# Kernel tuning notes

Measured on AMD Instinct MI355X. Metric: run time of the kernel, lower is better.

The kernel has to match this reference:

```python
import jax, jax.numpy as jnp
import numpy as np

N_EMBD = 1024
N_HEAD = 16
HEAD_SIZE = N_EMBD // N_HEAD


def setup_inputs() -> dict:
    key = jax.random.key(0)
    k_x, k_w, k_b = jax.random.split(key, 3)
    B, T, C = 2, 2048, N_EMBD
    x = jax.random.normal(k_x, (B, T, C), dtype=jnp.float32)
    # Linear(n_embd, 3*n_embd): weight [C, 3C] (applied as x @ W), bias [3C]
    w_qkv = jax.random.normal(k_w, (C, 3 * C), dtype=jnp.float32) * (1.0 / np.sqrt(C))
    b_qkv = jax.random.normal(k_b, (3 * C,), dtype=jnp.float32) * 0.02
    return {"x": x, "w_qkv": w_qkv, "b_qkv": b_qkv}


def reference(x, w_qkv, b_qkv):
    B, T, C = x.shape
    H, D = N_HEAD, HEAD_SIZE
    qkv = x @ w_qkv + b_qkv                      # [B, T, 3C]
    q, k, v = jnp.split(qkv, 3, axis=-1)         # each [B, T, C]
    # [B, T, C] -> [B, H, T, D]
    q = q.reshape(B, T, H, D).transpose(0, 2, 1, 3)
    k = k.reshape(B, T, H, D).transpose(0, 2, 1, 3)
    v = v.reshape(B, T, H, D).transpose(0, 2, 1, 3)
    scores = jnp.einsum('bhqd,bhkd->bhqk', q, k) / jnp.sqrt(jnp.float32(D))
    causal = jnp.tril(jnp.ones((T, T), dtype=bool))  # allow j <= i
    scores = jnp.where(causal[None, None, :, :], scores, -jnp.inf)
    weights = jax.nn.softmax(scores, axis=-1)    # [B, H, T, T]
    out = jnp.einsum('bhqk,bhkd->bhqd', weights, v)
    out = out.transpose(0, 2, 1, 3).reshape(B, T, C)
    return out
```

## Files before the change

### kernel.cpp

```cpp
#include <hip/hip_runtime.h>
#include <hip/hip_bf16.h>


#define CDIM  1024
#define C3    3072
#define HS    64
#define TLEN  2048
#define KVT   64
#define SCL   0.1803368801111204f

typedef __attribute__((ext_vector_type(8))) short bf16x8;
typedef __attribute__((ext_vector_type(4))) float f32x4;
typedef __attribute__((ext_vector_type(4))) unsigned short u16x4;

__device__ __forceinline__ unsigned short f2b(float f) {
    unsigned u = __float_as_uint(f);
    unsigned r = (u + 0x7FFFu + ((u >> 16) & 1u)) >> 16;
    return (unsigned short)r;
}
__device__ __forceinline__ float b2f(unsigned short u) {
    return __uint_as_float(((unsigned)u) << 16);
}
__device__ __forceinline__ float fexp2(float x) {
    return __builtin_amdgcn_exp2f(x);
}
__device__ __forceinline__ unsigned pkbf(float a, float b) {
    float2 f; f.x = a; f.y = b;
    __hip_bfloat162 h = __float22bfloat162_rn(f);
    union { __hip_bfloat162 h2; unsigned u; } c;
    c.h2 = h;
    return c.u;
}
__device__ __forceinline__ void gl_lds16(const unsigned short* g, unsigned short* l) {
    __builtin_amdgcn_global_load_lds((const __attribute__((address_space(1))) void*)g,
                                     (__attribute__((address_space(3))) void*)l, 16, 0, 0);
}
__device__ __forceinline__ int detect_bf(const void* bias, int lane) {
    unsigned w = ((const unsigned*)bias)[lane];
    unsigned e = (w >> 7) & 0xFF;
    unsigned long long m = __ballot(e >= 100 && e <= 135);
    return __popcll(m) >= 48;
}

__device__ __forceinline__ void plswap(unsigned x, unsigned& y0, unsigned& y1) {
    unsigned aa = x, bb = x;
    asm("v_permlane32_swap_b32 %0, %1" : "+v"(aa), "+v"(bb));
    asm("v_permlane16_swap_b32 %0, %1" : "+v"(aa), "+v"(bb));
    y0 = aa; y1 = bb;
}
__device__ __forceinline__ bf16x8 xfrag(unsigned x00, unsigned x01,
                                        unsigned x10, unsigned x11, int qsel) {
    unsigned y000, y100, y001, y101, y010, y110, y011, y111;
    plswap(x00, y000, y100);
    plswap(x01, y001, y101);
    plswap(x10, y010, y110);
    plswap(x11, y011, y111);
    union { unsigned u[4]; bf16x8 v; } r;
    r.u[0] = qsel ? y010 : y000;
    r.u[1] = qsel ? y011 : y001;
    r.u[2] = qsel ? y110 : y100;
    r.u[3] = qsel ? y111 : y101;
    return r.v;
}

__global__ __launch_bounds__(256) void k_prep(const void* __restrict__ w,
                                              const void* __restrict__ x,
                                              const void* __restrict__ bias,
                                              unsigned short* __restrict__ wt,
                                              unsigned short* __restrict__ xb) {
    __shared__ unsigned short tile[64 * 66];
    int t = threadIdx.x;
    int isbf = detect_bf(bias, t & 63);
    int bid = blockIdx.x;

    {
        int n0 = (bid % 48) * 64;
        int k0 = (bid / 48) * 64;
        for (int i = 0; i < 16; ++i) {
            int idx = t + i * 256;
            int r = idx >> 6, c = idx & 63;
            unsigned short v;
            if (isbf) v = ((const unsigned short*)w)[(k0 + r) * C3 + n0 + c];
            else      v = f2b(((const float*)w)[(k0 + r) * C3 + n0 + c]);
            tile[r * 66 + c] = v;
        }
        __syncthreads();
        for (int i = 0; i < 16; ++i) {
            int idx = t + i * 256;
            int r = idx >> 6, c = idx & 63;
            wt[(n0 + r) * CDIM + k0 + c] = tile[c * 66 + r];
        }
    }
    if (!isbf) {
        const float4* s = (const float4*)x;
        uint2* d = (uint2*)xb;
        for (int sb = bid; sb < 2048; sb += 768) {
            int base = sb * 512;
            for (int j = t; j < 512; j += 256) {
                float4 v = s[base + j];
                uint2 o_;
                o_.x = (unsigned)f2b(v.x) | ((unsigned)f2b(v.y) << 16);
                o_.y = (unsigned)f2b(v.z) | ((unsigned)f2b(v.w) << 16);
                d[base + j] = o_;
            }
        }
    }
}

__global__ __launch_bounds__(256, 3) void k_gemm_qkv(const void* __restrict__ xraw,
                                                     const unsigned short* __restrict__ xb,
                                                     const void* __restrict__ biasraw,
                                                     const unsigned short* __restrict__ Bt,
                                                     unsigned short* __restrict__ qk,
                                                     unsigned short* __restrict__ k2,
                                                     unsigned short* __restrict__ v2) {
    __shared__ __align__(16) unsigned short As[2 * 128 * 32];
    __shared__ __align__(16) unsigned short Bs[2 * 128 * 32];
    int tid  = threadIdx.x;
    int lane = tid & 63, wv = tid >> 6;
    int quad = lane >> 4, l16 = lane & 15;
    int isbf = detect_bf(biasraw, lane);
    const unsigned short* A = isbf ? (const unsigned short*)xraw : xb;

    int lin = blockIdx.x + 24 * blockIdx.y;
    int swz = (lin & 7) * 96 + (lin >> 3);
    int m0 = (swz / 24) * 128, n0 = (swz % 24) * 128;
    int wm = (wv >> 1) * 64, wn = (wv & 1) * 64;

    f32x4 acc[4][4] = {};

    int r0 = tid >> 2;
    int g0 = (((tid & 3) ^ (r0 & 3)) * 8);
    const unsigned short* a0 = A  + (m0 + r0) * CDIM + g0;
    const unsigned short* b0 = Bt + (n0 + r0) * CDIM + g0;
    unsigned short* dA = As + tid * 8;
    unsigned short* dB = Bs + tid * 8;

    int sw4 = l16 & 3;
    int aro = (wm + l16) * 32 + ((quad ^ sw4) * 8);
    int bro = (wn + l16) * 32 + ((quad ^ sw4) * 8);

    gl_lds16(a0,                 dA);
    gl_lds16(a0 + 64 * CDIM,     dA + 2048);
    gl_lds16(b0,                 dB);
    gl_lds16(b0 + 64 * CDIM,     dB + 2048);
    gl_lds16(a0 + 32,            dA + 4096);
    gl_lds16(a0 + 64 * CDIM + 32, dA + 4096 + 2048);
    gl_lds16(b0 + 32,            dB + 4096);
    gl_lds16(b0 + 64 * CDIM + 32, dB + 4096 + 2048);
    asm volatile("s_waitcnt vmcnt(4)" ::: "memory");
    __builtin_amdgcn_s_barrier();

    #pragma unroll 2
    for (int kt = 0; kt < 32; ++kt) {
        int cur = kt & 1;
        const unsigned short* Ac = As + cur * 4096;
        const unsigned short* Bc = Bs + cur * 4096;

        bf16x8 af[4], bfv[4];
        #pragma unroll
        for (int mt = 0; mt < 4; ++mt)
            af[mt] = *(const bf16x8*)&Ac[aro + mt * 512];
        #pragma unroll
        for (int nt = 0; nt < 4; ++nt)
            bfv[nt] = *(const bf16x8*)&Bc[bro + nt * 512];

        __builtin_amdgcn_s_setprio(1);
        #pragma unroll
        for (int mt = 0; mt < 4; ++mt)
            #pragma unroll
            for (int nt = 0; nt < 4; ++nt)
                acc[mt][nt] = __builtin_amdgcn_mfma_f32_16x16x32_bf16(af[mt], bfv[nt], acc[mt][nt], 0, 0, 0);
        __builtin_amdgcn_s_setprio(0);

        __builtin_amdgcn_s_barrier();
        if (kt < 30) {
            int koff = (kt + 2) * 32;
            unsigned short* tA = As + cur * 4096;
            unsigned short* tB = Bs + cur * 4096;
            gl_lds16(a0 + koff,            tA + tid * 8);
            gl_lds16(a0 + 64 * CDIM + koff, tA + tid * 8 + 2048);
            gl_lds16(b0 + koff,            tB + tid * 8);
            gl_lds16(b0 + 64 * CDIM + koff, tB + tid * 8 + 2048);
            asm volatile("s_waitcnt vmcnt(4)" ::: "memory");
        } else {
            asm volatile("s_waitcnt vmcnt(0)" ::: "memory");
        }
        __builtin_amdgcn_s_barrier();
    }

    if (n0 < 1024) {
        for (int mt = 0; mt < 4; ++mt) {
            int row = m0 + wm + mt * 16 + quad * 4;
            for (int nt = 0; nt < 4; ++nt) {
                int col = n0 + wn + nt * 16 + l16;
                float bv = isbf ? b2f(((const unsigned short*)biasraw)[col])
                                : ((const float*)biasraw)[col];
                for (int i = 0; i < 4; ++i)
                    qk[(row + i) * 2048 + col] = f2b(acc[mt][nt][i] + bv);
            }
        }
    } else if (n0 < 2048) {
        for (int mt = 0; mt < 4; ++mt) {
            int row = m0 + wm + mt * 16 + quad * 4;
            int tq = row & 2047, b = row >> 11;
            for (int nt = 0; nt < 4; ++nt) {
                int col = n0 + wn + nt * 16 + l16;
                float bv = isbf ? b2f(((const unsigned short*)biasraw)[col])
                                : ((const float*)biasraw)[col];
                int c = col - 1024;
                int hh = c >> 6, d = c & 63;
                int base = ((b * 16 + hh) * 32 + (tq >> 6)) * 4096
                         + ((tq >> 5) & 1) * 2048 + ((tq >> 4) & 1) * 1024
                         + (d >> 5) * 512 + ((d >> 3) & 3) * 128
                         + (tq & 15) * 8 + (d & 7);
                for (int i = 0; i < 4; ++i)
                    k2[base + i * 8] = f2b(acc[mt][nt][i] + bv);
            }
        }
    } else {
        for (int mt = 0; mt < 4; ++mt) {
            int row = m0 + wm + mt * 16 + quad * 4;
            int tq = row & 2047, b = row >> 11;
            for (int nt = 0; nt < 4; ++nt) {
                int col = n0 + wn + nt * 16 + l16;
                float bv = isbf ? b2f(((const unsigned short*)biasraw)[col])
                                : ((const float*)biasraw)[col];
                int c = col - 2048;
                int hh = c >> 6, d = c & 63;
                int base = ((b * 16 + hh) * 32 + (tq >> 6)) * 4096
                         + ((tq >> 5) & 1) * 2048 + (d >> 4) * 512
                         + ((tq >> 3) & 3) * 128 + (d & 15) * 8 + (tq & 7);
                u16x4 pk;
                for (int i = 0; i < 4; ++i) pk[i] = f2b(acc[mt][nt][i] + bv);
                *(u16x4*)&v2[base] = pk;
            }
        }
    }
}

__global__ __launch_bounds__(256, 3) void k_attn(const unsigned short* __restrict__ qk,
                                                 const unsigned short* __restrict__ k2,
                                                 const unsigned short* __restrict__ v2,
                                                 const void* __restrict__ biasraw,
                                                 void* __restrict__ outv) {
    __shared__ __align__(16) float SMf[4416];

    int tid  = threadIdx.x;
    int lane = tid & 63, wv = tid >> 6;
    int quad = lane >> 4, l16 = lane & 15;
    int isbf = detect_bf(biasraw, lane);
    int bh = blockIdx.x;
    int g  = 31 - blockIdx.y;
    int b = bh >> 4, h = bh & 15;
    int rowbase = b * TLEN;

    int s_ = wv >> 1;
    int p  = wv & 1;
    int qbase = 64 * g + 32 * s_;
    int T  = g + 1;
    int Tw = T - ((s_ == 0 && p == 1) ? 1 : 0);
    bool dmw = (p == s_);

    bf16x8 qf[2][2];
    for (int qt = 0; qt < 2; ++qt)
        for (int kh = 0; kh < 2; ++kh)
            qf[qt][kh] = *(const bf16x8*)&qk[(rowbase + qbase + qt * 16 + l16) * 2048
                                            + h * HS + kh * 32 + quad * 8];

    f32x4 o[2][4] = {};
    float ls[2] = {0.f, 0.f};

    const unsigned short* kp = k2 + bh * 131072 + p * 2048 + lane * 8;
    const unsigned short* vp = v2 + bh * 131072 + p * 2048 + lane * 8;

    bf16x8 kf00, kf01, kf10, kf11;
    f32x4 svA[2][2], svB[2][2];
    {
        bf16x8 k0a = *(const bf16x8*)kp;
        bf16x8 k0b = *(const bf16x8*)(kp + 512);
        bf16x8 k0c = *(const bf16x8*)(kp + 1024);
        bf16x8 k0d = *(const bf16x8*)(kp + 1536);
        kp += 4096;
        kf00 = *(const bf16x8*)kp;
        kf01 = *(const bf16x8*)(kp + 512);
        kf10 = *(const bf16x8*)(kp + 1024);
        kf11 = *(const bf16x8*)(kp + 1536);
        kp += 4096;
        #pragma unroll
        for (int qt = 0; qt < 2; ++qt) {
            f32x4 z0 = {};
            z0 = __builtin_amdgcn_mfma_f32_16x16x32_bf16(k0a, qf[qt][0], z0, 0, 0, 0);
            z0 = __builtin_amdgcn_mfma_f32_16x16x32_bf16(k0b, qf[qt][1], z0, 0, 0, 0);
            svA[qt][0] = z0;
            f32x4 z1 = {};
            z1 = __builtin_amdgcn_mfma_f32_16x16x32_bf16(k0c, qf[qt][0], z1, 0, 0, 0);
            z1 = __builtin_amdgcn_mfma_f32_16x16x32_bf16(k0d, qf[qt][1], z1, 0, 0, 0);
            svA[qt][1] = z1;
        }
    }

    auto trip = [&](f32x4 (&svin)[2][2], f32x4 (&svout)[2][2], int tt) {
        bf16x8 av0 = *(const bf16x8*)vp;
        bf16x8 av1 = *(const bf16x8*)(vp + 512);
        bf16x8 av2 = *(const bf16x8*)(vp + 1024);
        bf16x8 av3 = *(const bf16x8*)(vp + 1536);
        vp += 4096;

        __builtin_amdgcn_s_setprio(1);
        #pragma unroll
        for (int qt = 0; qt < 2; ++qt) {
            f32x4 z0 = {};
            z0 = __builtin_amdgcn_mfma_f32_16x16x32_bf16(kf00, qf[qt][0], z0, 0, 0, 0);
            z0 = __builtin_amdgcn_mfma_f32_16x16x32_bf16(kf01, qf[qt][1], z0, 0, 0, 0);
            svout[qt][0] = z0;
            f32x4 z1 = {};
            z1 = __builtin_amdgcn_mfma_f32_16x16x32_bf16(kf10, qf[qt][0], z1, 0, 0, 0);
            z1 = __builtin_amdgcn_mfma_f32_16x16x32_bf16(kf11, qf[qt][1], z1, 0, 0, 0);
            svout[qt][1] = z1;
        }
        __builtin_amdgcn_s_setprio(0);

        kf00 = *(const bf16x8*)kp;
        kf01 = *(const bf16x8*)(kp + 512);
        kf10 = *(const bf16x8*)(kp + 1024);
        kf11 = *(const bf16x8*)(kp + 1536);
        kp += 4096;

        unsigned sp[2][2][2];
        int kvb = tt * KVT + 32 * p;
        if (dmw && tt == T - 1) {
            #pragma unroll
            for (int qt = 0; qt < 2; ++qt) {
                float psum = 0.f;
                int q = qbase + qt * 16 + l16;
                #pragma unroll
                for (int nt = 0; nt < 2; ++nt) {
                    float pv[4];
                    #pragma unroll
                    for (int i = 0; i < 4; ++i) {
                        float arg = fmaf(svin[qt][nt][i], SCL, -12.0f);
                        int kv = kvb + nt * 16 + quad * 4 + i;
                        if (kv > q) arg = -1e30f;
                        pv[i] = fexp2(arg);
                        psum += pv[i];
                    }
                    sp[qt][nt][0] = pkbf(pv[0], pv[1]);
                    sp[qt][nt][1] = pkbf(pv[2], pv[3]);
                }
                ls[qt] += psum;
            }
        } else {
            #pragma unroll
            for (int qt = 0; qt < 2; ++qt) {
                float psum = 0.f;
                #pragma unroll
                for (int nt = 0; nt < 2; ++nt) {
                    float pv[4];
                    #pragma unroll
                    for (int i = 0; i < 4; ++i) {
                        float arg = fmaf(svin[qt][nt][i], SCL, -12.0f);
                        pv[i] = fexp2(arg);
                        psum += pv[i];
                    }
                    sp[qt][nt][0] = pkbf(pv[0], pv[1]);
                    sp[qt][nt][1] = pkbf(pv[2], pv[3]);
                }
                ls[qt] += psum;
            }
        }

        int qsel = quad & 2;
        bf16x8 f0 = xfrag(sp[0][0][0], sp[0][0][1], sp[0][1][0], sp[0][1][1], qsel);
        bf16x8 f1 = xfrag(sp[1][0][0], sp[1][0][1], sp[1][1][0], sp[1][1][1], qsel);
        __builtin_amdgcn_s_setprio(1);
        o[0][0] = __builtin_amdgcn_mfma_f32_16x16x32_bf16(av0, f0, o[0][0], 0, 0, 0);
        o[1][0] = __builtin_amdgcn_mfma_f32_16x16x32_bf16(av0, f1, o[1][0], 0, 0, 0);
        o[0][1] = __builtin_amdgcn_mfma_f32_16x16x32_bf16(av1, f0, o[0][1], 0, 0, 0);
        o[1][1] = __builtin_amdgcn_mfma_f32_16x16x32_bf16(av1, f1, o[1][1], 0, 0, 0);
        o[0][2] = __builtin_amdgcn_mfma_f32_16x16x32_bf16(av2, f0, o[0][2], 0, 0, 0);
        o[1][2] = __builtin_amdgcn_mfma_f32_16x16x32_bf16(av2, f1, o[1][2], 0, 0, 0);
        o[0][3] = __builtin_amdgcn_mfma_f32_16x16x32_bf16(av3, f0, o[0][3], 0, 0, 0);
        o[1][3] = __builtin_amdgcn_mfma_f32_16x16x32_bf16(av3, f1, o[1][3], 0, 0, 0);
        __builtin_amdgcn_s_setprio(0);
    };

    int t = 0;
    for (; t + 2 <= Tw; t += 2) {
        trip(svA, svB, t);
        trip(svB, svA, t + 1);
    }
    if (t < Tw) trip(svA, svB, t);

    #pragma unroll
    for (int qt = 0; qt < 2; ++qt) {
        ls[qt] += __shfl_xor(ls[qt], 16);
        ls[qt] += __shfl_xor(ls[qt], 32);
    }
    float* mrg  = SMf;
    float* lbuf = SMf + 4352;

    if (p == 1) {
        #pragma unroll
        for (int qt = 0; qt < 2; ++qt)
            #pragma unroll
            for (int dt = 0; dt < 4; ++dt)
                *(f32x4*)&mrg[s_ * (32 * 68) + (qt * 16 + l16) * 68 + dt * 16 + quad * 4] = o[qt][dt];
        if (quad == 0) {
            lbuf[s_ * 32 + l16]      = ls[0];
            lbuf[s_ * 32 + 16 + l16] = ls[1];
        }
    }
    __syncthreads();
    if (p == 0) {
        #pragma unroll
        for (int qt = 0; qt < 2; ++qt) {
            float lt = ls[qt] + lbuf[s_ * 32 + qt * 16 + l16];
            float inv = 1.0f / lt;
            int q = qbase + qt * 16 + l16;
            if (isbf) {
                unsigned short* out = (unsigned short*)outv;
                #pragma unroll
                for (int dt = 0; dt < 4; ++dt) {
                    f32x4 m = *(const f32x4*)&mrg[s_ * (32 * 68) + (qt * 16 + l16) * 68 + dt * 16 + quad * 4];
                    u16x4 ov;
                    #pragma unroll
                    for (int i = 0; i < 4; ++i) ov[i] = f2b((o[qt][dt][i] + m[i]) * inv);
                    *(u16x4*)&out[(rowbase + q) * CDIM + h * HS + dt * 16 + quad * 4] = ov;
                }
            } else {
                float* out = (float*)outv;
                #pragma unroll
                for (int dt = 0; dt < 4; ++dt) {
                    f32x4 m = *(const f32x4*)&mrg[s_ * (32 * 68) + (qt * 16 + l16) * 68 + dt * 16 + quad * 4];
                    float4 ov;
                    ov.x = (o[qt][dt][0] + m[0]) * inv;
                    ov.y = (o[qt][dt][1] + m[1]) * inv;
                    ov.z = (o[qt][dt][2] + m[2]) * inv;
                    ov.w = (o[qt][dt][3] + m[3]) * inv;
                    *(float4*)&out[(rowbase + q) * CDIM + h * HS + dt * 16 + quad * 4] = ov;
                }
            }
        }
    }
}

extern "C" void kernel_launch(void* const* d_in, const int* in_sizes, int n_in,
                              void* d_out, int out_size, void* d_ws, size_t ws_size,
                              hipStream_t stream) {
    const void* x    = d_in[0];
    const void* w    = d_in[1];
    const void* bias = d_in[2];

    char* ws = (char*)d_ws;
    unsigned short* xb  = (unsigned short*)ws;
    unsigned short* wt  = (unsigned short*)(ws + (8u  << 20));
    unsigned short* qk  = (unsigned short*)(ws + (16u << 20));
    unsigned short* k2  = (unsigned short*)(ws + (32u << 20));
    unsigned short* v2  = (unsigned short*)(ws + (40u << 20));

    k_prep<<<768, 256, 0, stream>>>(w, x, bias, wt, xb);
    k_gemm_qkv<<<dim3(24, 32), 256, 0, stream>>>(x, xb, bias, wt, qk, k2, v2);
    k_attn<<<dim3(32, 32), 256, 0, stream>>>(qk, k2, v2, bias, d_out);
}
```

Measured before the change: 148.6 us.

## Enlarge QKV GEMM tiles to 256x256 with 8 waves and interleaved prefetch

The QKV projection GEMM moves from 128x128 tiles (256 threads, K-step 32) to 256x256 tiles (512 threads, K-step 64), with each wave holding an 8x4 grid of MFMA accumulators. The main loop is split into four MFMA phases with barriers in between. The A and B global-to-LDS loads for the next K-step are issued in separate phases so they overlap with compute. The goal is more data reuse per LDS byte and better load/compute overlap. The cost is only 192 workgroups, and the roughly 128 KB of LDS per block likely allows one block per CU, so part of the GPU may sit idle.

Result: slower. 156.4 us (+5.2%).

```diff
diff --git a/kernel.cpp b/kernel.cpp
--- a/kernel.cpp
+++ b/kernel.cpp
@@ -107,93 +107,140 @@
     }
 }
 
-__global__ __launch_bounds__(256, 3) void k_gemm_qkv(const void* __restrict__ xraw,
+__global__ __launch_bounds__(512, 2) void k_gemm_qkv(const void* __restrict__ xraw,
                                                      const unsigned short* __restrict__ xb,
                                                      const void* __restrict__ biasraw,
                                                      const unsigned short* __restrict__ Bt,
                                                      unsigned short* __restrict__ qk,
                                                      unsigned short* __restrict__ k2,
                                                      unsigned short* __restrict__ v2) {
-    __shared__ __align__(16) unsigned short As[2 * 128 * 32];
-    __shared__ __align__(16) unsigned short Bs[2 * 128 * 32];
+    __shared__ __align__(16) unsigned short As[2 * 16384];
+    __shared__ __align__(16) unsigned short Bs[2 * 16384];
     int tid  = threadIdx.x;
     int lane = tid & 63, wv = tid >> 6;
     int quad = lane >> 4, l16 = lane & 15;
     int isbf = detect_bf(biasraw, lane);
     const unsigned short* A = isbf ? (const unsigned short*)xraw : xb;
 
-    int lin = blockIdx.x + 24 * blockIdx.y;
-    int swz = (lin & 7) * 96 + (lin >> 3);
-    int m0 = (swz / 24) * 128, n0 = (swz % 24) * 128;
-    int wm = (wv >> 1) * 64, wn = (wv & 1) * 64;
-
-    f32x4 acc[4][4] = {};
-
-    int r0 = tid >> 2;
-    int g0 = (((tid & 3) ^ (r0 & 3)) * 8);
-    const unsigned short* a0 = A  + (m0 + r0) * CDIM + g0;
-    const unsigned short* b0 = Bt + (n0 + r0) * CDIM + g0;
-    unsigned short* dA = As + tid * 8;
-    unsigned short* dB = Bs + tid * 8;
-
-    int sw4 = l16 & 3;
-    int aro = (wm + l16) * 32 + ((quad ^ sw4) * 8);
-    int bro = (wn + l16) * 32 + ((quad ^ sw4) * 8);
-
-    gl_lds16(a0,                 dA);
-    gl_lds16(a0 + 64 * CDIM,     dA + 2048);
-    gl_lds16(b0,                 dB);
-    gl_lds16(b0 + 64 * CDIM,     dB + 2048);
-    gl_lds16(a0 + 32,            dA + 4096);
-    gl_lds16(a0 + 64 * CDIM + 32, dA + 4096 + 2048);
-    gl_lds16(b0 + 32,            dB + 4096);
-    gl_lds16(b0 + 64 * CDIM + 32, dB + 4096 + 2048);
-    asm volatile("s_waitcnt vmcnt(4)" ::: "memory");
+    int lin = blockIdx.x;
+    int swz = (lin & 7) * 24 + (lin >> 3);
+    int m0 = (swz / 12) * 256, n0 = (swz % 12) * 256;
+    int wr = wv >> 2, wc = wv & 3;
+
+    f32x4 acc[8][4] = {};
+
+    int r0 = tid >> 3;
+    int c0 = (((tid & 7) ^ (r0 & 7)) * 8);
+    const unsigned short* aS0 = A  + (m0 + r0) * CDIM + c0;
+    const unsigned short* aS1 = aS0 + 128 * CDIM;
+    const unsigned short* bS0 = Bt + (n0 + r0) * CDIM + c0;
+    const unsigned short* bS1 = bS0 + 128 * CDIM;
+
+    int sw8 = l16 & 7;
+    int arow = (wr * 128 + l16) * 64;
+    int brow = (wc * 64  + l16) * 64;
+    int kc0 = ((quad)     ^ sw8) * 8;
+    int kc1 = ((4 + quad) ^ sw8) * 8;
+
+    gl_lds16(aS0,             As + tid * 8);
+    gl_lds16(aS0 + 64 * CDIM, As + tid * 8 + 4096);
+    gl_lds16(aS1,             As + 8192 + tid * 8);
+    gl_lds16(aS1 + 64 * CDIM, As + 8192 + tid * 8 + 4096);
+    gl_lds16(bS0,             Bs + tid * 8);
+    gl_lds16(bS0 + 64 * CDIM, Bs + tid * 8 + 4096);
+    gl_lds16(bS1,             Bs + 8192 + tid * 8);
+    gl_lds16(bS1 + 64 * CDIM, Bs + 8192 + tid * 8 + 4096);
+    asm volatile("s_waitcnt vmcnt(0)" ::: "memory");
     __builtin_amdgcn_s_barrier();
 
-    #pragma unroll 2
-    for (int kt = 0; kt < 32; ++kt) {
+    for (int kt = 0; kt < 16; ++kt) {
         int cur = kt & 1;
-        const unsigned short* Ac = As + cur * 4096;
-        const unsigned short* Bc = Bs + cur * 4096;
-
-        bf16x8 af[4], bfv[4];
-        #pragma unroll
-        for (int mt = 0; mt < 4; ++mt)
-            af[mt] = *(const bf16x8*)&Ac[aro + mt * 512];
+        const unsigned short* Ac = As + cur * 16384;
+        const unsigned short* Bc = Bs + cur * 16384;
+        unsigned short* Anx = As + (cur ^ 1) * 16384;
+        unsigned short* Bnx = Bs + (cur ^ 1) * 16384;
+        bool st = (kt < 15);
+        int kof = (kt + 1) * 64;
+
+        bf16x8 afr[4], bfv0[4];
+        #pragma unroll
+        for (int mt = 0; mt < 4; ++mt)
+            afr[mt] = *(const bf16x8*)&Ac[arow + mt * 1024 + kc0];
         #pragma unroll
         for (int nt = 0; nt < 4; ++nt)
-            bfv[nt] = *(const bf16x8*)&Bc[bro + nt * 512];
-
+            bfv0[nt] = *(const bf16x8*)&Bc[brow + nt * 1024 + kc0];
+        if (st) {
+            gl_lds16(aS0 + kof,             Anx + tid * 8);
+            gl_lds16(aS0 + 64 * CDIM + kof, Anx + tid * 8 + 4096);
+            gl_lds16(aS1 + kof,             Anx + 8192 + tid * 8);
+            gl_lds16(aS1 + 64 * CDIM + kof, Anx + 8192 + tid * 8 + 4096);
+        }
+        __builtin_amdgcn_s_barrier();
         __builtin_amdgcn_s_setprio(1);
         #pragma unroll
         for (int mt = 0; mt < 4; ++mt)
             #pragma unroll
             for (int nt = 0; nt < 4; ++nt)
-                acc[mt][nt] = __builtin_amdgcn_mfma_f32_16x16x32_bf16(af[mt], bfv[nt], acc[mt][nt], 0, 0, 0);
+                acc[mt][nt] = __builtin_amdgcn_mfma_f32_16x16x32_bf16(afr[mt], bfv0[nt], acc[mt][nt], 0, 0, 0);
         __builtin_amdgcn_s_setprio(0);
-
-        __builtin_amdgcn_s_barrier();
-        if (kt < 30) {
-            int koff = (kt + 2) * 32;
-            unsigned short* tA = As + cur * 4096;
-            unsigned short* tB = Bs + cur * 4096;
-            gl_lds16(a0 + koff,            tA + tid * 8);
-            gl_lds16(a0 + 64 * CDIM + koff, tA + tid * 8 + 2048);
-            gl_lds16(b0 + koff,            tB + tid * 8);
-            gl_lds16(b0 + 64 * CDIM + koff, tB + tid * 8 + 2048);
-            asm volatile("s_waitcnt vmcnt(4)" ::: "memory");
-        } else {
-            asm volatile("s_waitcnt vmcnt(0)" ::: "memory");
-        }
+        __builtin_amdgcn_s_barrier();
+
+        #pragma unroll
+        for (int mt = 0; mt < 4; ++mt)
+            afr[mt] = *(const bf16x8*)&Ac[arow + (4 + mt) * 1024 + kc0];
+        if (st) {
+            gl_lds16(bS0 + kof,             Bnx + tid * 8);
+            gl_lds16(bS0 + 64 * CDIM + kof, Bnx + tid * 8 + 4096);
+            gl_lds16(bS1 + kof,             Bnx + 8192 + tid * 8);
+            gl_lds16(bS1 + 64 * CDIM + kof, Bnx + 8192 + tid * 8 + 4096);
+        }
+        __builtin_amdgcn_s_barrier();
+        __builtin_amdgcn_s_setprio(1);
+        #pragma unroll
+        for (int mt = 0; mt < 4; ++mt)
+            #pragma unroll
+            for (int nt = 0; nt < 4; ++nt)
+                acc[4 + mt][nt] = __builtin_amdgcn_mfma_f32_16x16x32_bf16(afr[mt], bfv0[nt], acc[4 + mt][nt], 0, 0, 0);
+        __builtin_amdgcn_s_setprio(0);
+        __builtin_amdgcn_s_barrier();
+
+        bf16x8 bfv1[4];
+        #pragma unroll
+        for (int mt = 0; mt < 4; ++mt)
+            afr[mt] = *(const bf16x8*)&Ac[arow + mt * 1024 + kc1];
+        #pragma unroll
+        for (int nt = 0; nt < 4; ++nt)
+            bfv1[nt] = *(const bf16x8*)&Bc[brow + nt * 1024 + kc1];
+        __builtin_amdgcn_s_barrier();
+        __builtin_amdgcn_s_setprio(1);
+        #pragma unroll
+        for (int mt = 0; mt < 4; ++mt)
+            #pragma unroll
+            for (int nt = 0; nt < 4; ++nt)
+                acc[mt][nt] = __builtin_amdgcn_mfma_f32_16x16x32_bf16(afr[mt], bfv1[nt], acc[mt][nt], 0, 0, 0);
+        __builtin_amdgcn_s_setprio(0);
+        __builtin_amdgcn_s_barrier();
+
+        #pragma unroll
+        for (int mt = 0; mt < 4; ++mt)
+            afr[mt] = *(const bf16x8*)&Ac[arow + (4 + mt) * 1024 + kc1];
+        __builtin_amdgcn_s_barrier();
+        __builtin_amdgcn_s_setprio(1);
+        #pragma unroll
+        for (int mt = 0; mt < 4; ++mt)
+            #pragma unroll
+            for (int nt = 0; nt < 4; ++nt)
+                acc[4 + mt][nt] = __builtin_amdgcn_mfma_f32_16x16x32_bf16(afr[mt], bfv1[nt], acc[4 + mt][nt], 0, 0, 0);
+        __builtin_amdgcn_s_setprio(0);
+        asm volatile("s_waitcnt vmcnt(0)" ::: "memory");
         __builtin_amdgcn_s_barrier();
     }
 
     if (n0 < 1024) {
-        for (int mt = 0; mt < 4; ++mt) {
-            int row = m0 + wm + mt * 16 + quad * 4;
+        for (int mt = 0; mt < 8; ++mt) {
+            int row = m0 + wr * 128 + mt * 16 + quad * 4;
             for (int nt = 0; nt < 4; ++nt) {
-                int col = n0 + wn + nt * 16 + l16;
+                int col = n0 + wc * 64 + nt * 16 + l16;
                 float bv = isbf ? b2f(((const unsigned short*)biasraw)[col])
                                 : ((const float*)biasraw)[col];
                 for (int i = 0; i < 4; ++i)
@@ -201,11 +248,11 @@
             }
         }
     } else if (n0 < 2048) {
-        for (int mt = 0; mt < 4; ++mt) {
-            int row = m0 + wm + mt * 16 + quad * 4;
+        for (int mt = 0; mt < 8; ++mt) {
+            int row = m0 + wr * 128 + mt * 16 + quad * 4;
             int tq = row & 2047, b = row >> 11;
             for (int nt = 0; nt < 4; ++nt) {
-                int col = n0 + wn + nt * 16 + l16;
+                int col = n0 + wc * 64 + nt * 16 + l16;
                 float bv = isbf ? b2f(((const unsigned short*)biasraw)[col])
                                 : ((const float*)biasraw)[col];
                 int c = col - 1024;
@@ -219,11 +266,11 @@
             }
         }
     } else {
-        for (int mt = 0; mt < 4; ++mt) {
-            int row = m0 + wm + mt * 16 + quad * 4;
+        for (int mt = 0; mt < 8; ++mt) {
+            int row = m0 + wr * 128 + mt * 16 + quad * 4;
             int tq = row & 2047, b = row >> 11;
             for (int nt = 0; nt < 4; ++nt) {
-                int col = n0 + wn + nt * 16 + l16;
+                int col = n0 + wc * 64 + nt * 16 + l16;
                 float bv = isbf ? b2f(((const unsigned short*)biasraw)[col])
                                 : ((const float*)biasraw)[col];
                 int c = col - 2048;
@@ -460,6 +507,6 @@
     unsigned short* v2  = (unsigned short*)(ws + (40u << 20));
 
     k_prep<<<768, 256, 0, stream>>>(w, x, bias, wt, xb);
-    k_gemm_qkv<<<dim3(24, 32), 256, 0, stream>>>(x, xb, bias, wt, qk, k2, v2);
+    k_gemm_qkv<<<192, 512, 0, stream>>>(x, xb, bias, wt, qk, k2, v2);
     k_attn<<<dim3(32, 32), 256, 0, stream>>>(qk, k2, v2, bias, d_out);
 }
```
